# Performance work log

Measured on AMD Instinct MI355X. Metric: run time of the kernel, lower is better.

Reference implementation:

```python
import jax, jax.numpy as jnp
import numpy as np

KSIZE = (2, 2)


def setup_inputs() -> dict:
    key = jax.random.key(0)
    k1, k2 = jax.random.split(key)
    B, H, W, C = 32, 128, 128, 64
    oy, ox = H * KSIZE[0], W * KSIZE[1]
    total = B * oy * ox * C
    x = jax.random.normal(k1, (B, H, W, C), dtype=jnp.float32)
    ind = jax.random.randint(k2, (B, H, W, C), 0, total, dtype=jnp.int64)
    return {"input": x, "ind": ind}


def reference(input, ind):
    # Max-unpooling: scatter pooled values into a zero-initialized buffer of
    # shape [B, H*ky, W*kx, C] at the flat positions given by `ind`.
    # tf.scatter_nd sums on duplicate indices -> .at[].add matches exactly.
    B, H, W, C = input.shape
    oy, ox = H * KSIZE[0], W * KSIZE[1]
    total = B * oy * ox * C
    flat = jnp.zeros((total,), dtype=input.dtype).at[ind.reshape(-1)].add(
        input.reshape(-1)
    )
    return flat.reshape(B, oy, ox, C)
```

## Files before the change

kernel.cpp:

```cpp
#include <hip/hip_runtime.h>


typedef float    f32x4 __attribute__((ext_vector_type(4)));
typedef int      i32x4 __attribute__((ext_vector_type(4)));
typedef unsigned u32x2 __attribute__((ext_vector_type(2)));

#define N_TOT   (1 << 25)
#define OUT_TOT (1 << 27)
#define T1      1024
#define PT      (N_TOT / T1)
#define PT4     (PT / 4)
#define NB1     1024
#define CSH     17
#define CAP     36864
#define SSH     15
#define NSUB    4
#define WFL     32768
#define BATCH   16384
#define KREG    72

__global__ __launch_bounds__(1024) void k_scatter(const float* __restrict__ x,
                                                  const int* __restrict__ ind,
                                                  unsigned* __restrict__ gcur,
                                                  u32x2* __restrict__ P1) {
  __shared__ u32x2    sbuf[BATCH];
  __shared__ unsigned hist[NB1], sbase[NB1], alloc[NB1];
  const int t = blockIdx.x;
  const i32x4* pi = reinterpret_cast<const i32x4*>(ind) + (size_t)t * PT4;
  const f32x4* pv = reinterpret_cast<const f32x4*>(x)  + (size_t)t * PT4;

  for (int bt = 0; bt < 2; ++bt) {
    const int v0 = bt * (BATCH / 4);
    i32x4 idx[4];
    f32x4 val[4];
    #pragma unroll
    for (int q = 0; q < 4; ++q) {
      idx[q] = __builtin_nontemporal_load(pi + v0 + q * 1024 + threadIdx.x);
      val[q] = __builtin_nontemporal_load(pv + v0 + q * 1024 + threadIdx.x);
    }
    hist[threadIdx.x] = 0;
    __syncthreads();
    unsigned r[16];
    #pragma unroll
    for (int q = 0; q < 4; ++q) {
      r[4 * q + 0] = atomicAdd(&hist[(unsigned)idx[q].x >> CSH], 1u);
      r[4 * q + 1] = atomicAdd(&hist[(unsigned)idx[q].y >> CSH], 1u);
      r[4 * q + 2] = atomicAdd(&hist[(unsigned)idx[q].z >> CSH], 1u);
      r[4 * q + 3] = atomicAdd(&hist[(unsigned)idx[q].w >> CSH], 1u);
    }
    __syncthreads();
    alloc[threadIdx.x] = atomicAdd(&gcur[threadIdx.x], hist[threadIdx.x]);
    if (threadIdx.x < 64) {
      const unsigned lane = threadIdx.x;
      unsigned h[16], sum = 0;
      #pragma unroll
      for (int j = 0; j < 16; ++j) { h[j] = hist[16 * lane + j]; sum += h[j]; }
      unsigned inc = sum;
      for (int off = 1; off < 64; off <<= 1) {
        unsigned o = __shfl_up(inc, off, 64);
        if (lane >= (unsigned)off) inc += o;
      }
      unsigned exc = inc - sum;
      #pragma unroll
      for (int j = 0; j < 16; ++j) { sbase[16 * lane + j] = exc; exc += h[j]; }
    }
    __syncthreads();
    #pragma unroll
    for (int q = 0; q < 4; ++q) {
      sbuf[sbase[(unsigned)idx[q].x >> CSH] + r[4 * q + 0]] =
          (u32x2){__float_as_uint(val[q].x), (unsigned)idx[q].x};
      sbuf[sbase[(unsigned)idx[q].y >> CSH] + r[4 * q + 1]] =
          (u32x2){__float_as_uint(val[q].y), (unsigned)idx[q].y};
      sbuf[sbase[(unsigned)idx[q].z >> CSH] + r[4 * q + 2]] =
          (u32x2){__float_as_uint(val[q].z), (unsigned)idx[q].z};
      sbuf[sbase[(unsigned)idx[q].w >> CSH] + r[4 * q + 3]] =
          (u32x2){__float_as_uint(val[q].w), (unsigned)idx[q].w};
    }
    __syncthreads();
    #pragma unroll
    for (int k = 0; k < BATCH / 1024; ++k) {
      unsigned j = (unsigned)(k * 1024 + threadIdx.x);
      u32x2 q = sbuf[j];
      unsigned b = q.y >> CSH;
      unsigned pos = alloc[b] + (j - sbase[b]);
      if (pos < CAP)
        P1[(size_t)b * CAP + pos] = q;
    }
    __syncthreads();
  }
}

__global__ __launch_bounds__(512, 2) void k_waccum(const u32x2* __restrict__ P1,
                                                   const unsigned* __restrict__ gcur,
                                                   float* __restrict__ out) {
  __shared__ float w[WFL];
  const int c = blockIdx.x;
  const unsigned len = min(gcur[c], (unsigned)CAP);
  const u32x2* P = P1 + (size_t)c * CAP;
  u32x2 p[KREG];
  #pragma unroll
  for (int k = 0; k < KREG; ++k) {
    unsigned j = (unsigned)(k * 512) + threadIdx.x;
    p[k] = (j < len) ? __builtin_nontemporal_load(P + j)
                     : (u32x2){0u, 0xFFFFFFFFu};
  }
  f32x4* w4 = reinterpret_cast<f32x4*>(w);
  for (int sub = 0; sub < NSUB; ++sub) {
    const unsigned key = ((unsigned)c << 2) | (unsigned)sub;
    for (int i = threadIdx.x; i < WFL / 4; i += 512) w4[i] = (f32x4){0.f, 0.f, 0.f, 0.f};
    __syncthreads();
    #pragma unroll
    for (int k = 0; k < KREG; ++k) {
      if ((p[k].y >> SSH) == key)
        atomicAdd(&w[p[k].y & (WFL - 1)], __uint_as_float(p[k].x));
    }
    __syncthreads();
    f32x4* o = reinterpret_cast<f32x4*>(out + ((size_t)c << CSH) + ((size_t)sub << SSH));
    for (int i = threadIdx.x; i < WFL / 4; i += 512)
      __builtin_nontemporal_store(w4[i], o + i);
    __syncthreads();
  }
}

__global__ __launch_bounds__(256) void unpool_scatter_kernel(
    const float* __restrict__ x, const int* __restrict__ ind,
    float* __restrict__ out, int n4) {
  int i = blockIdx.x * blockDim.x + threadIdx.x;
  if (i >= n4) return;
  f32x4 v  = reinterpret_cast<const f32x4*>(x)[i];
  i32x4 id = reinterpret_cast<const i32x4*>(ind)[i];
  unsafeAtomicAdd(&out[id.x], v.x);
  unsafeAtomicAdd(&out[id.y], v.y);
  unsafeAtomicAdd(&out[id.z], v.z);
  unsafeAtomicAdd(&out[id.w], v.w);
}

extern "C" void kernel_launch(void* const* d_in, const int* in_sizes, int n_in,
                              void* d_out, int out_size, void* d_ws, size_t ws_size,
                              hipStream_t stream) {
  const float* x   = (const float*)d_in[0];
  const int*   ind = (const int*)d_in[1];
  float*       out = (float*)d_out;
  const int n = in_sizes[0];

  const size_t szG  = ((size_t)NB1 * sizeof(unsigned) + 255) & ~(size_t)255;
  const size_t szP1 = (size_t)NB1 * CAP * sizeof(u32x2);
  const size_t need = szG + szP1;

  const bool shape_ok = (n == N_TOT) && (out_size == OUT_TOT);

  if (!shape_ok || ws_size < need) {
    (void)hipMemsetAsync(d_out, 0, (size_t)out_size * sizeof(float), stream);
    const int n4 = n / 4;
    unpool_scatter_kernel<<<(n4 + 255) / 256, 256, 0, stream>>>(x, ind, out, n4);
    return;
  }

  char* ws = (char*)d_ws;
  unsigned* gcur = (unsigned*)ws;
  u32x2*    P1   = (u32x2*)(ws + szG);

  (void)hipMemsetAsync(gcur, 0, (size_t)NB1 * sizeof(unsigned), stream);
  k_scatter<<<T1,  1024, 0, stream>>>(x, ind, gcur, P1);
  k_waccum <<<NB1,  512, 0, stream>>>(P1, gcur, out);
}
```

Baseline: 379.0 us.

## Split bucket records into float values and 16-bit local offsets with finer buckets

Buckets now cover 64K output elements each, and there are twice as many of them. This lets the intermediate record drop from an 8-byte (value, full index) pair to a 4-byte value plus a 2-byte local offset, stored in separate arrays. The goal is to cut the global write and read traffic of the bucketed intermediate between the scatter and accumulate kernels, and to halve the per-thread register arrays in the accumulate pass. In exchange there are two narrow scattered store streams instead of one 8-byte store, larger shared histogram and prefix arrays in the scatter kernel, and less slack in per-bucket capacity.

```diff
diff --git a/kernel.cpp b/kernel.cpp
--- a/kernel.cpp
+++ b/kernel.cpp
@@ -10,19 +10,19 @@
 #define T1      1024
 #define PT      (N_TOT / T1)
 #define PT4     (PT / 4)
-#define NB1     1024
-#define CSH     17
-#define CAP     36864
-#define SSH     15
-#define NSUB    4
+#define NB1     2048
+#define CSH     16
+#define CAP     17408
+#define NSUB    2
 #define WFL     32768
 #define BATCH   16384
-#define KREG    72
+#define KREG    34
 
 __global__ __launch_bounds__(1024) void k_scatter(const float* __restrict__ x,
                                                   const int* __restrict__ ind,
                                                   unsigned* __restrict__ gcur,
-                                                  u32x2* __restrict__ P1) {
+                                                  float* __restrict__ P1v,
+                                                  unsigned short* __restrict__ P1l) {
   __shared__ u32x2    sbuf[BATCH];
   __shared__ unsigned hist[NB1], sbase[NB1], alloc[NB1];
   const int t = blockIdx.x;
@@ -39,6 +39,7 @@
       val[q] = __builtin_nontemporal_load(pv + v0 + q * 1024 + threadIdx.x);
     }
     hist[threadIdx.x] = 0;
+    hist[threadIdx.x + 1024] = 0;
     __syncthreads();
     unsigned r[16];
     #pragma unroll
@@ -50,11 +51,13 @@
     }
     __syncthreads();
     alloc[threadIdx.x] = atomicAdd(&gcur[threadIdx.x], hist[threadIdx.x]);
+    alloc[threadIdx.x + 1024] =
+        atomicAdd(&gcur[threadIdx.x + 1024], hist[threadIdx.x + 1024]);
     if (threadIdx.x < 64) {
       const unsigned lane = threadIdx.x;
-      unsigned h[16], sum = 0;
+      unsigned h[32], sum = 0;
       #pragma unroll
-      for (int j = 0; j < 16; ++j) { h[j] = hist[16 * lane + j]; sum += h[j]; }
+      for (int j = 0; j < 32; ++j) { h[j] = hist[32 * lane + j]; sum += h[j]; }
       unsigned inc = sum;
       for (int off = 1; off < 64; off <<= 1) {
         unsigned o = __shfl_up(inc, off, 64);
@@ -62,7 +65,7 @@
       }
       unsigned exc = inc - sum;
       #pragma unroll
-      for (int j = 0; j < 16; ++j) { sbase[16 * lane + j] = exc; exc += h[j]; }
+      for (int j = 0; j < 32; ++j) { sbase[32 * lane + j] = exc; exc += h[j]; }
     }
     __syncthreads();
     #pragma unroll
@@ -83,39 +86,48 @@
       u32x2 q = sbuf[j];
       unsigned b = q.y >> CSH;
       unsigned pos = alloc[b] + (j - sbase[b]);
-      if (pos < CAP)
-        P1[(size_t)b * CAP + pos] = q;
+      if (pos < CAP) {
+        P1v[(size_t)b * CAP + pos] = __uint_as_float(q.x);
+        P1l[(size_t)b * CAP + pos] = (unsigned short)(q.y & 0xFFFFu);
+      }
     }
     __syncthreads();
   }
 }
 
-__global__ __launch_bounds__(512, 2) void k_waccum(const u32x2* __restrict__ P1,
+__global__ __launch_bounds__(512, 2) void k_waccum(const float* __restrict__ P1v,
+                                                   const unsigned short* __restrict__ P1l,
                                                    const unsigned* __restrict__ gcur,
                                                    float* __restrict__ out) {
   __shared__ float w[WFL];
   const int c = blockIdx.x;
   const unsigned len = min(gcur[c], (unsigned)CAP);
-  const u32x2* P = P1 + (size_t)c * CAP;
-  u32x2 p[KREG];
+  const float* Pv = P1v + (size_t)c * CAP;
+  const unsigned short* Pl = P1l + (size_t)c * CAP;
+  float    pv[KREG];
+  unsigned pl[KREG];
   #pragma unroll
   for (int k = 0; k < KREG; ++k) {
     unsigned j = (unsigned)(k * 512) + threadIdx.x;
-    p[k] = (j < len) ? __builtin_nontemporal_load(P + j)
-                     : (u32x2){0u, 0xFFFFFFFFu};
+    if (j < len) {
+      pv[k] = Pv[j];
+      pl[k] = (unsigned)Pl[j];
+    } else {
+      pv[k] = 0.0f;
+      pl[k] = 0u;
+    }
   }
   f32x4* w4 = reinterpret_cast<f32x4*>(w);
   for (int sub = 0; sub < NSUB; ++sub) {
-    const unsigned key = ((unsigned)c << 2) | (unsigned)sub;
     for (int i = threadIdx.x; i < WFL / 4; i += 512) w4[i] = (f32x4){0.f, 0.f, 0.f, 0.f};
     __syncthreads();
     #pragma unroll
     for (int k = 0; k < KREG; ++k) {
-      if ((p[k].y >> SSH) == key)
-        atomicAdd(&w[p[k].y & (WFL - 1)], __uint_as_float(p[k].x));
+      if ((pl[k] >> 15) == (unsigned)sub)
+        atomicAdd(&w[pl[k] & (WFL - 1)], pv[k]);
     }
     __syncthreads();
-    f32x4* o = reinterpret_cast<f32x4*>(out + ((size_t)c << CSH) + ((size_t)sub << SSH));
+    f32x4* o = reinterpret_cast<f32x4*>(out + ((size_t)c << CSH) + ((size_t)sub << 15));
     for (int i = threadIdx.x; i < WFL / 4; i += 512)
       __builtin_nontemporal_store(w4[i], o + i);
     __syncthreads();
@@ -144,8 +156,9 @@
   const int n = in_sizes[0];
 
   const size_t szG  = ((size_t)NB1 * sizeof(unsigned) + 255) & ~(size_t)255;
-  const size_t szP1 = (size_t)NB1 * CAP * sizeof(u32x2);
-  const size_t need = szG + szP1;
+  const size_t szPv = (size_t)NB1 * CAP * sizeof(float);
+  const size_t szPl = (size_t)NB1 * CAP * sizeof(unsigned short);
+  const size_t need = szG + szPv + szPl;
 
   const bool shape_ok = (n == N_TOT) && (out_size == OUT_TOT);
 
@@ -157,10 +170,11 @@
   }
 
   char* ws = (char*)d_ws;
-  unsigned* gcur = (unsigned*)ws;
-  u32x2*    P1   = (u32x2*)(ws + szG);
+  unsigned*       gcur = (unsigned*)ws;
+  float*          P1v  = (float*)(ws + szG);
+  unsigned short* P1l  = (unsigned short*)(ws + szG + szPv);
 
   (void)hipMemsetAsync(gcur, 0, (size_t)NB1 * sizeof(unsigned), stream);
-  k_scatter<<<T1,  1024, 0, stream>>>(x, ind, gcur, P1);
-  k_waccum <<<NB1,  512, 0, stream>>>(P1, gcur, out);
+  k_scatter<<<T1,  1024, 0, stream>>>(x, ind, gcur, P1v, P1l);
+  k_waccum <<<NB1,  512, 0, stream>>>(P1v, P1l, gcur, out);
 }
```

After: 423.8 us. +11.8%, slower.
